# Kernel tuning notes

Hardware: AMD Instinct MI355X
Metric: run time of the kernel (lower is better)

## Reference

```python
import jax, jax.numpy as jnp
import numpy as np

B, T, C = 4, 2048, 1024
H, HS = 16, 64


def setup_inputs() -> dict:
    key = jax.random.key(0)
    ks = jax.random.split(key, 5)
    scale = (H * C) ** (-0.5)
    x = jax.random.normal(ks[0], (B, T, C), dtype=jnp.float32)
    Wk = jax.random.normal(ks[1], (H, C, HS), dtype=jnp.float32) * scale
    Wq = jax.random.normal(ks[2], (H, C, HS), dtype=jnp.float32) * scale
    Wv = jax.random.normal(ks[3], (H, C, HS), dtype=jnp.float32) * scale
    proj_w = jax.random.normal(ks[4], (C, C), dtype=jnp.float32) / C ** 0.5
    proj_b = jnp.zeros((C,), dtype=jnp.float32)
    return {"x": x, "Wk": Wk, "Wq": Wq, "Wv": Wv, "proj_w": proj_w, "proj_b": proj_b}


def reference(x, Wk, Wq, Wv, proj_w, proj_b):
    b, t, c = x.shape
    # per-head projections: (B,T,C) x (H,C,D) -> (B,H,T,D)
    q = jnp.einsum('btc,hcd->bhtd', x, Wq)
    k = jnp.einsum('btc,hcd->bhtd', x, Wk)
    v = jnp.einsum('btc,hcd->bhtd', x, Wv)
    # NOTE: original module does not scale by 1/sqrt(head_size)
    wei = jnp.einsum('bhtd,bhsd->bhts', q, k)  # (B,H,T,T)
    causal = jnp.tril(jnp.ones((t, t), dtype=bool))
    wei = jnp.where(causal, wei, -jnp.inf)
    wei = jax.nn.softmax(wei, axis=-1)
    out = jnp.einsum('bhts,bhsd->bhtd', wei, v)
    out = out.transpose(0, 2, 1, 3).reshape(b, t, c)  # concat heads
    return out @ proj_w + proj_b
```

## Files before the change

kernel.cpp:

```cpp
#include <hip/hip_runtime.h>

typedef unsigned short u16;
typedef u16 u16x4 __attribute__((ext_vector_type(4)));
typedef u16 u16x8 __attribute__((ext_vector_type(8)));
typedef unsigned u32x2 __attribute__((ext_vector_type(2)));
typedef __bf16 bf16x8 __attribute__((ext_vector_type(8)));
typedef float f32x4 __attribute__((ext_vector_type(4)));

#define DEV static __device__ __forceinline__

DEV u16 f2bf(float f) {
  union { float f; unsigned u; } v; v.f = f;
  return (u16)((v.u + 0x7FFFu + ((v.u >> 16) & 1u)) >> 16);
}

DEV unsigned pack2(float a, float b) {
  unsigned ua = __builtin_bit_cast(unsigned, a) + 0x8000u;
  unsigned ub = __builtin_bit_cast(unsigned, b) + 0x8000u;
  return (ua >> 16) | (ub & 0xFFFF0000u);
}

DEV void async16(const void* g, void* l) {
  __builtin_amdgcn_global_load_lds((const __attribute__((address_space(1))) void*)g,
                                   (__attribute__((address_space(3))) void*)l, 16, 0, 0);
}

DEV f32x4 mfma16(bf16x8 a, bf16x8 b, f32x4 c) {
  return __builtin_amdgcn_mfma_f32_16x16x32_bf16(a, b, c, 0, 0, 0);
}

DEV float exp2fast(float x) { return __builtin_amdgcn_exp2f(x); }

__global__ __launch_bounds__(256) void k_pack_x(const float* __restrict__ x,
                                                u16* __restrict__ o) {
  int i = (blockIdx.x * 256 + threadIdx.x) * 4;
  float4 v = *(const float4*)(x + i);
  u16x4 t = { f2bf(v.x), f2bf(v.y), f2bf(v.z), f2bf(v.w) };
  *(u16x4*)(o + i) = t;
}

__global__ __launch_bounds__(256) void k_tpack(const float* __restrict__ src,
                                               u16* __restrict__ dst,
                                               int rows, int cols, float scale) {
  __shared__ float t[64 * 72];
  const int tid = threadIdx.x;
  src += (size_t)blockIdx.z * rows * cols;
  dst += (size_t)blockIdx.z * rows * cols;
  const int c0 = blockIdx.x * 64, r0 = blockIdx.y * 64;
  const int rr = tid >> 2, cb = (tid & 3) * 16;
  const float* s = src + (size_t)(r0 + rr) * cols + c0 + cb;
  float4 v0 = *(const float4*)(s + 0);
  float4 v1 = *(const float4*)(s + 4);
  float4 v2 = *(const float4*)(s + 8);
  float4 v3 = *(const float4*)(s + 12);
  *(float4*)(t + rr * 72 + cb + 0)  = v0;
  *(float4*)(t + rr * 72 + cb + 4)  = v1;
  *(float4*)(t + rr * 72 + cb + 8)  = v2;
  *(float4*)(t + rr * 72 + cb + 12) = v3;
  __syncthreads();
  const int dd = tid >> 2, eb = (tid & 3) * 16;
  u16x8 o0, o1;
#pragma unroll
  for (int e = 0; e < 8; ++e) o0[e] = f2bf(t[(eb + e) * 72 + dd] * scale);
#pragma unroll
  for (int e = 0; e < 8; ++e) o1[e] = f2bf(t[(eb + 8 + e) * 72 + dd] * scale);
  u16* dp = dst + (size_t)(c0 + dd) * rows + r0 + eb;
  *(u16x8*)dp = o0;
  *(u16x8*)(dp + 8) = o1;
}

template <int MODE>
__global__ __launch_bounds__(256) void k_gemm(const u16* __restrict__ A,
                                              const u16* __restrict__ Bt,
                                              u16* __restrict__ qd,
                                              u16* __restrict__ kd,
                                              u16* __restrict__ vd,
                                              float* __restrict__ out,
                                              const float* __restrict__ bias) {
  __shared__ u16 As[128 * 32];
  __shared__ u16 Bs[128 * 32];
  const int tid = threadIdx.x;
  const int wave = tid >> 6, lane = tid & 63;
  const int quad = lane >> 4, l15 = lane & 15;
  const int wm = wave & 1, wn = wave >> 1;
  const size_t mb = blockIdx.y, nb = blockIdx.x;
  const u16* ga = A + (mb * 128 + (tid >> 2)) * 1024 + (tid & 3) * 8;
  const u16* gb = Bt + (nb * 128 + (tid >> 2)) * 1024 + (tid & 3) * 8;
  f32x4 acc[4][4] = {};
  for (int k0 = 0; k0 < 1024; k0 += 32) {
    async16(ga,             As + wave * 512);
    async16(ga + 64 * 1024, As + 2048 + wave * 512);
    async16(gb,             Bs + wave * 512);
    async16(gb + 64 * 1024, Bs + 2048 + wave * 512);
    ga += 32; gb += 32;
    __syncthreads();
    bf16x8 af[4], bf[4];
#pragma unroll
    for (int i = 0; i < 4; ++i)
      af[i] = *(const bf16x8*)(As + (wm * 64 + i * 16 + l15) * 32 + quad * 8);
#pragma unroll
    for (int j = 0; j < 4; ++j)
      bf[j] = *(const bf16x8*)(Bs + (wn * 64 + j * 16 + l15) * 32 + quad * 8);
#pragma unroll
    for (int i = 0; i < 4; ++i)
#pragma unroll
      for (int j = 0; j < 4; ++j)
        acc[i][j] = mfma16(af[i], bf[j], acc[i][j]);
    __syncthreads();
  }
  const size_t m0 = mb * 128 + wm * 64;
  const int n0 = (int)nb * 128 + wn * 64;
  if (MODE == 0) {
#pragma unroll
    for (int j = 0; j < 4; ++j) {
      const int n = n0 + j * 16 + l15;
      const int p = n >> 10, hh = (n >> 6) & 15, d = n & 63;
      if (p == 2) {
#pragma unroll
        for (int i = 0; i < 4; ++i) {
          const size_t m = m0 + i * 16 + quad * 4;
          const size_t bb = m >> 11, tt = m & 2047;
          u16x4 pk = { f2bf(acc[i][j][0]), f2bf(acc[i][j][1]),
                       f2bf(acc[i][j][2]), f2bf(acc[i][j][3]) };
          *(u16x4*)(vd + ((bb * 16 + hh) * 64 + d) * 2048 + tt) = pk;
        }
      } else {
        u16* dst = (p == 0) ? qd : kd;
#pragma unroll
        for (int i = 0; i < 4; ++i)
#pragma unroll
          for (int r = 0; r < 4; ++r) {
            const size_t m = m0 + i * 16 + quad * 4 + r;
            const size_t bb = m >> 11, tt = m & 2047;
            dst[((bb * 16 + hh) * 2048 + tt) * 64 + d] = f2bf(acc[i][j][r]);
          }
      }
    }
  } else {
#pragma unroll
    for (int j = 0; j < 4; ++j) {
      const int n = n0 + j * 16 + l15;
      const float bv = bias[n];
#pragma unroll
      for (int i = 0; i < 4; ++i)
#pragma unroll
        for (int r = 0; r < 4; ++r) {
          const size_t m = m0 + i * 16 + quad * 4 + r;
          out[m * 1024 + n] = acc[i][j][r] + bv;
        }
    }
  }
}

__global__ __launch_bounds__(256) void k_attn(const u16* __restrict__ Qg,
                                              const u16* __restrict__ Kg,
                                              const u16* __restrict__ Vtg,
                                              u16* __restrict__ Og) {
  __shared__ u16 Kbuf[2 * 4096];
  __shared__ u16 Vbuf[2 * 4096];
  __shared__ u16 Pbuf[4 * 32 * 72];
  const int tid = threadIdx.x;
  const int wave = tid >> 6, lane = tid & 63;
  const int quad = lane >> 4, l15 = lane & 15;
  const int quad4 = quad * 4, quad8 = quad * 8;
  const int bh = blockIdx.x;
  const int qpair = blockIdx.y;
  const u16* kg = Kg + (size_t)bh * 2048 * 64;
  const u16* vg = Vtg + (size_t)bh * 64 * 2048;
  u16* Pw = Pbuf + wave * (32 * 72);
  const int b = bh >> 4, h = bh & 15;

  const int lrow = lane >> 3;
  const int lchunk = ((lane & 7) ^ lrow) << 3;
  const u16* kst = kg + (size_t)(wave * 16 + lrow) * 64 + lchunk;
  const u16* vst = vg + (size_t)(wave * 16 + lrow) * 2048 + lchunk;
  u16* kdst0 = Kbuf + wave * 1024;
  u16* vdst0 = Vbuf + wave * 1024;

  const int rowoff = l15 * 64;
  const int swz0 = ((0 + quad) ^ (l15 & 7)) << 3;
  const int swz1 = ((4 + quad) ^ (l15 & 7)) << 3;

  for (int half = 0; half < 2; ++half) {
    const int qb = half ? (15 - qpair) : qpair;
    const int qlo = qb * 128 + wave * 32;
    const int ntw = 2 * qb + 1 + (wave >> 1);
    const int ntb = 2 * qb + 2;
    const u16* qg = Qg + ((size_t)bh * 2048 + (size_t)qb * 128) * 64;

    bf16x8 qf[2][2];
#pragma unroll
    for (int i = 0; i < 2; ++i)
#pragma unroll
      for (int c = 0; c < 2; ++c)
        qf[i][c] = *(const bf16x8*)(qg + (size_t)(wave * 32 + i * 16 + l15) * 64 +
                                    c * 32 + quad8);

    f32x4 oacc[2][4] = {};
    float lsum[2] = {0.f, 0.f};

    {
      async16(kst, kdst0);
      async16(kst + 512, kdst0 + 512);
      async16(vst, vdst0);
      async16(vst + 16384, vdst0 + 512);
    }

    for (int it = 0; it < ntb; ++it) {
      __syncthreads();

      if (it + 1 < ntb) {
        const int buf = (it + 1) & 1;
        const size_t s0 = (size_t)(it + 1) * 64;
        async16(kst + s0 * 64,        kdst0 + buf * 4096);
        async16(kst + s0 * 64 + 512,  kdst0 + buf * 4096 + 512);
        async16(vst + s0,             vdst0 + buf * 4096);
        async16(vst + s0 + 16384,     vdst0 + buf * 4096 + 512);
      }

      if (it < ntw) {
        const int s0 = it * 64;
        const u16* Kb = Kbuf + (it & 1) * 4096;
        const u16* Vb = Vbuf + (it & 1) * 4096;

        f32x4 sacc[4][2] = {};
#pragma unroll
        for (int j = 0; j < 4; ++j) {
          bf16x8 kf0 = *(const bf16x8*)(Kb + j * 1024 + rowoff + swz0);
          bf16x8 kf1 = *(const bf16x8*)(Kb + j * 1024 + rowoff + swz1);
          sacc[j][0] = mfma16(kf0, qf[0][0], sacc[j][0]);
          sacc[j][0] = mfma16(kf1, qf[0][1], sacc[j][0]);
          sacc[j][1] = mfma16(kf0, qf[1][0], sacc[j][1]);
          sacc[j][1] = mfma16(kf1, qf[1][1], sacc[j][1]);
        }

#pragma unroll
        for (int j = 0; j < 4; ++j)
#pragma unroll
          for (int i = 0; i < 2; ++i)
#pragma unroll
            for (int r = 0; r < 4; ++r)
              sacc[j][i][r] = exp2fast(sacc[j][i][r]);

        if (it == ntw - 1) {
#pragma unroll
          for (int j = 0; j < 4; ++j)
#pragma unroll
            for (int i = 0; i < 2; ++i)
#pragma unroll
              for (int r = 0; r < 4; ++r)
                if (s0 + j * 16 + quad4 + r > qlo + i * 16 + l15) sacc[j][i][r] = 0.f;
        }

#pragma unroll
        for (int j = 0; j < 4; ++j)
#pragma unroll
          for (int i = 0; i < 2; ++i) {
            lsum[i] += (sacc[j][i][0] + sacc[j][i][1]) +
                       (sacc[j][i][2] + sacc[j][i][3]);
            u32x2 pk = { pack2(sacc[j][i][0], sacc[j][i][1]),
                         pack2(sacc[j][i][2], sacc[j][i][3]) };
            *(u32x2*)(Pw + (i * 16 + l15) * 72 + j * 16 + quad4) = pk;
          }

        bf16x8 pa[2][2];
#pragma unroll
        for (int i = 0; i < 2; ++i)
#pragma unroll
          for (int c = 0; c < 2; ++c)
            pa[i][c] = *(const bf16x8*)(Pw + (i * 16 + l15) * 72 + c * 32 + quad8);

#pragma unroll
        for (int n = 0; n < 4; ++n) {
          bf16x8 vf0 = *(const bf16x8*)(Vb + n * 1024 + rowoff + swz0);
          bf16x8 vf1 = *(const bf16x8*)(Vb + n * 1024 + rowoff + swz1);
          oacc[0][n] = mfma16(pa[0][0], vf0, oacc[0][n]);
          oacc[0][n] = mfma16(pa[0][1], vf1, oacc[0][n]);
          oacc[1][n] = mfma16(pa[1][0], vf0, oacc[1][n]);
          oacc[1][n] = mfma16(pa[1][1], vf1, oacc[1][n]);
        }
      }
    }

#pragma unroll
    for (int i = 0; i < 2; ++i) {
      lsum[i] += __shfl_xor(lsum[i], 16, 64);
      lsum[i] += __shfl_xor(lsum[i], 32, 64);
    }
#pragma unroll
    for (int i = 0; i < 2; ++i)
#pragma unroll
      for (int r = 0; r < 4; ++r) {
        const float inv = 1.0f / __shfl(lsum[i], quad4 + r, 16);
        const size_t t = (size_t)qb * 128 + wave * 32 + i * 16 + quad4 + r;
#pragma unroll
        for (int n = 0; n < 4; ++n)
          Og[((size_t)b * 2048 + t) * 1024 + h * 64 + n * 16 + l15] =
              f2bf(oacc[i][n][r] * inv);
      }

    __syncthreads();
  }
}

extern "C" void kernel_launch(void* const* d_in, const int* in_sizes, int n_in,
                              void* d_out, int out_size, void* d_ws, size_t ws_size,
                              hipStream_t stream) {
  const float* x  = (const float*)d_in[0];
  const float* Wk = (const float*)d_in[1];
  const float* Wq = (const float*)d_in[2];
  const float* Wv = (const float*)d_in[3];
  const float* pw = (const float*)d_in[4];
  const float* pb = (const float*)d_in[5];
  float* out = (float*)d_out;
  char* ws = (char*)d_ws;

  u16* xb  = (u16*)(ws + 0);
  u16* wT  = (u16*)(ws + 16777216);
  u16* pwT = (u16*)(ws + 23068672);
  u16* q   = (u16*)(ws + 25165824);
  u16* kb  = (u16*)(ws + 41943040);
  u16* vt  = (u16*)(ws + 58720256);
  u16* att = (u16*)(ws + 0);

  const float LOG2E = 1.44269504088896340736f;
  k_pack_x<<<8192, 256, 0, stream>>>(x, xb);
  k_tpack<<<dim3(1, 16, 16), 256, 0, stream>>>(Wq, wT + 0,           1024, 64, LOG2E);
  k_tpack<<<dim3(1, 16, 16), 256, 0, stream>>>(Wk, wT + 1024 * 1024, 1024, 64, 1.0f);
  k_tpack<<<dim3(1, 16, 16), 256, 0, stream>>>(Wv, wT + 2048 * 1024, 1024, 64, 1.0f);
  k_tpack<<<dim3(16, 16, 1), 256, 0, stream>>>(pw, pwT, 1024, 1024, 1.0f);
  k_gemm<0><<<dim3(24, 64), 256, 0, stream>>>(xb, wT, q, kb, vt, nullptr, nullptr);
  k_attn<<<dim3(64, 8), 256, 0, stream>>>(q, kb, vt, att);
  k_gemm<1><<<dim3(8, 64), 256, 0, stream>>>(att, pwT, nullptr, nullptr, nullptr, out, pb);
}
```

Before: 269.3 us.

## Process four query blocks per attention workgroup sharing one K/V stream

Each attention workgroup now handles four causal-balanced query blocks (a, a+4, 11-a, 15-a) at once instead of two sequentially. Every K/V tile is loaded from global memory and LDS a single time and reused across all four query blocks, cutting redundant K/V traffic. The cost is half as many workgroups (256 over 256 CUs), heavy register pressure from four sets of accumulators and Q fragments (hence launch_bounds(256,1)), and possible spills or lower occupancy.

After: 285.8 us. +6.1%, slower.

```diff
diff --git a/kernel.cpp b/kernel.cpp
--- a/kernel.cpp
+++ b/kernel.cpp
@@ -152,10 +152,10 @@
   }
 }
 
-__global__ __launch_bounds__(256) void k_attn(const u16* __restrict__ Qg,
-                                              const u16* __restrict__ Kg,
-                                              const u16* __restrict__ Vtg,
-                                              u16* __restrict__ Og) {
+__global__ __launch_bounds__(256, 1) void k_attn(const u16* __restrict__ Qg,
+                                                 const u16* __restrict__ Kg,
+                                                 const u16* __restrict__ Vtg,
+                                                 u16* __restrict__ Og) {
   __shared__ u16 Kbuf[2 * 4096];
   __shared__ u16 Vbuf[2 * 4096];
   __shared__ u16 Pbuf[4 * 32 * 72];
@@ -164,9 +164,11 @@
   const int quad = lane >> 4, l15 = lane & 15;
   const int quad4 = quad * 4, quad8 = quad * 8;
   const int bh = blockIdx.x;
-  const int qpair = blockIdx.y;
+  const int a = blockIdx.y;
+  const int qbs[4] = { a, a + 4, 11 - a, 15 - a };
   const u16* kg = Kg + (size_t)bh * 2048 * 64;
   const u16* vg = Vtg + (size_t)bh * 64 * 2048;
+  const u16* qgb = Qg + (size_t)bh * 2048 * 64;
   u16* Pw = Pbuf + wave * (32 * 72);
   const int b = bh >> 4, h = bh & 15;
 
@@ -181,57 +183,65 @@
   const int swz0 = ((0 + quad) ^ (l15 & 7)) << 3;
   const int swz1 = ((4 + quad) ^ (l15 & 7)) << 3;
 
-  for (int half = 0; half < 2; ++half) {
-    const int qb = half ? (15 - qpair) : qpair;
-    const int qlo = qb * 128 + wave * 32;
-    const int ntw = 2 * qb + 1 + (wave >> 1);
-    const int ntb = 2 * qb + 2;
-    const u16* qg = Qg + ((size_t)bh * 2048 + (size_t)qb * 128) * 64;
-
-    bf16x8 qf[2][2];
+  bf16x8 qf[4][2][2];
+  int ntw[4], qlo[4];
+#pragma unroll
+  for (int z = 0; z < 4; ++z) {
+    qlo[z] = qbs[z] * 128 + wave * 32;
+    ntw[z] = 2 * qbs[z] + 1 + (wave >> 1);
 #pragma unroll
     for (int i = 0; i < 2; ++i)
 #pragma unroll
       for (int c = 0; c < 2; ++c)
-        qf[i][c] = *(const bf16x8*)(qg + (size_t)(wave * 32 + i * 16 + l15) * 64 +
-                                    c * 32 + quad8);
-
-    f32x4 oacc[2][4] = {};
-    float lsum[2] = {0.f, 0.f};
-
-    {
-      async16(kst, kdst0);
-      async16(kst + 512, kdst0 + 512);
-      async16(vst, vdst0);
-      async16(vst + 16384, vdst0 + 512);
-    }
-
-    for (int it = 0; it < ntb; ++it) {
-      __syncthreads();
-
-      if (it + 1 < ntb) {
-        const int buf = (it + 1) & 1;
-        const size_t s0 = (size_t)(it + 1) * 64;
-        async16(kst + s0 * 64,        kdst0 + buf * 4096);
-        async16(kst + s0 * 64 + 512,  kdst0 + buf * 4096 + 512);
-        async16(vst + s0,             vdst0 + buf * 4096);
-        async16(vst + s0 + 16384,     vdst0 + buf * 4096 + 512);
-      }
-
-      if (it < ntw) {
-        const int s0 = it * 64;
-        const u16* Kb = Kbuf + (it & 1) * 4096;
-        const u16* Vb = Vbuf + (it & 1) * 4096;
-
+        qf[z][i][c] = *(const bf16x8*)(qgb +
+            (size_t)(qbs[z] * 128 + wave * 32 + i * 16 + l15) * 64 + c * 32 + quad8);
+  }
+
+  f32x4 oacc[4][2][4] = {};
+  float lsum[4][2] = {};
+
+  const int ntb = 2 * (15 - a) + 2;
+
+  async16(kst, kdst0);
+  async16(kst + 512, kdst0 + 512);
+  async16(vst, vdst0);
+  async16(vst + 16384, vdst0 + 512);
+
+  for (int it = 0; it < ntb; ++it) {
+    __syncthreads();
+
+    if (it + 1 < ntb) {
+      const int buf = (it + 1) & 1;
+      const size_t s0n = (size_t)(it + 1) * 64;
+      async16(kst + s0n * 64,       kdst0 + buf * 4096);
+      async16(kst + s0n * 64 + 512, kdst0 + buf * 4096 + 512);
+      async16(vst + s0n,            vdst0 + buf * 4096);
+      async16(vst + s0n + 16384,    vdst0 + buf * 4096 + 512);
+    }
+
+    const int s0 = it * 64;
+    const u16* Kb = Kbuf + (it & 1) * 4096;
+    const u16* Vb = Vbuf + (it & 1) * 4096;
+
+    bf16x8 kf[4][2], vf[4][2];
+#pragma unroll
+    for (int j = 0; j < 4; ++j) {
+      kf[j][0] = *(const bf16x8*)(Kb + j * 1024 + rowoff + swz0);
+      kf[j][1] = *(const bf16x8*)(Kb + j * 1024 + rowoff + swz1);
+      vf[j][0] = *(const bf16x8*)(Vb + j * 1024 + rowoff + swz0);
+      vf[j][1] = *(const bf16x8*)(Vb + j * 1024 + rowoff + swz1);
+    }
+
+#pragma unroll
+    for (int z = 0; z < 4; ++z) {
+      if (it < ntw[z]) {
         f32x4 sacc[4][2] = {};
 #pragma unroll
         for (int j = 0; j < 4; ++j) {
-          bf16x8 kf0 = *(const bf16x8*)(Kb + j * 1024 + rowoff + swz0);
-          bf16x8 kf1 = *(const bf16x8*)(Kb + j * 1024 + rowoff + swz1);
-          sacc[j][0] = mfma16(kf0, qf[0][0], sacc[j][0]);
-          sacc[j][0] = mfma16(kf1, qf[0][1], sacc[j][0]);
-          sacc[j][1] = mfma16(kf0, qf[1][0], sacc[j][1]);
-          sacc[j][1] = mfma16(kf1, qf[1][1], sacc[j][1]);
+          sacc[j][0] = mfma16(kf[j][0], qf[z][0][0], sacc[j][0]);
+          sacc[j][0] = mfma16(kf[j][1], qf[z][0][1], sacc[j][0]);
+          sacc[j][1] = mfma16(kf[j][0], qf[z][1][0], sacc[j][1]);
+          sacc[j][1] = mfma16(kf[j][1], qf[z][1][1], sacc[j][1]);
         }
 
 #pragma unroll
@@ -242,22 +252,23 @@
             for (int r = 0; r < 4; ++r)
               sacc[j][i][r] = exp2fast(sacc[j][i][r]);
 
-        if (it == ntw - 1) {
+        if (it == ntw[z] - 1) {
 #pragma unroll
           for (int j = 0; j < 4; ++j)
 #pragma unroll
             for (int i = 0; i < 2; ++i)
 #pragma unroll
               for (int r = 0; r < 4; ++r)
-                if (s0 + j * 16 + quad4 + r > qlo + i * 16 + l15) sacc[j][i][r] = 0.f;
+                if (s0 + j * 16 + quad4 + r > qlo[z] + i * 16 + l15)
+                  sacc[j][i][r] = 0.f;
         }
 
 #pragma unroll
         for (int j = 0; j < 4; ++j)
 #pragma unroll
           for (int i = 0; i < 2; ++i) {
-            lsum[i] += (sacc[j][i][0] + sacc[j][i][1]) +
-                       (sacc[j][i][2] + sacc[j][i][3]);
+            lsum[z][i] += (sacc[j][i][0] + sacc[j][i][1]) +
+                          (sacc[j][i][2] + sacc[j][i][3]);
             u32x2 pk = { pack2(sacc[j][i][0], sacc[j][i][1]),
                          pack2(sacc[j][i][2], sacc[j][i][3]) };
             *(u32x2*)(Pw + (i * 16 + l15) * 72 + j * 16 + quad4) = pk;
@@ -272,34 +283,33 @@
 
 #pragma unroll
         for (int n = 0; n < 4; ++n) {
-          bf16x8 vf0 = *(const bf16x8*)(Vb + n * 1024 + rowoff + swz0);
-          bf16x8 vf1 = *(const bf16x8*)(Vb + n * 1024 + rowoff + swz1);
-          oacc[0][n] = mfma16(pa[0][0], vf0, oacc[0][n]);
-          oacc[0][n] = mfma16(pa[0][1], vf1, oacc[0][n]);
-          oacc[1][n] = mfma16(pa[1][0], vf0, oacc[1][n]);
-          oacc[1][n] = mfma16(pa[1][1], vf1, oacc[1][n]);
+          oacc[z][0][n] = mfma16(pa[0][0], vf[n][0], oacc[z][0][n]);
+          oacc[z][0][n] = mfma16(pa[0][1], vf[n][1], oacc[z][0][n]);
+          oacc[z][1][n] = mfma16(pa[1][0], vf[n][0], oacc[z][1][n]);
+          oacc[z][1][n] = mfma16(pa[1][1], vf[n][1], oacc[z][1][n]);
         }
       }
     }
-
+  }
+
+#pragma unroll
+  for (int z = 0; z < 4; ++z) {
 #pragma unroll
     for (int i = 0; i < 2; ++i) {
-      lsum[i] += __shfl_xor(lsum[i], 16, 64);
-      lsum[i] += __shfl_xor(lsum[i], 32, 64);
+      lsum[z][i] += __shfl_xor(lsum[z][i], 16, 64);
+      lsum[z][i] += __shfl_xor(lsum[z][i], 32, 64);
     }
 #pragma unroll
     for (int i = 0; i < 2; ++i)
 #pragma unroll
       for (int r = 0; r < 4; ++r) {
-        const float inv = 1.0f / __shfl(lsum[i], quad4 + r, 16);
-        const size_t t = (size_t)qb * 128 + wave * 32 + i * 16 + quad4 + r;
+        const float inv = 1.0f / __shfl(lsum[z][i], quad4 + r, 16);
+        const size_t t = (size_t)qbs[z] * 128 + wave * 32 + i * 16 + quad4 + r;
 #pragma unroll
         for (int n = 0; n < 4; ++n)
           Og[((size_t)b * 2048 + t) * 1024 + h * 64 + n * 16 + l15] =
-              f2bf(oacc[i][n][r] * inv);
+              f2bf(oacc[z][i][n][r] * inv);
       }
-
-    __syncthreads();
   }
 }
 
@@ -330,6 +340,6 @@
   k_tpack<<<dim3(1, 16, 16), 256, 0, stream>>>(Wv, wT + 2048 * 1024, 1024, 64, 1.0f);
   k_tpack<<<dim3(16, 16, 1), 256, 0, stream>>>(pw, pwT, 1024, 1024, 1.0f);
   k_gemm<0><<<dim3(24, 64), 256, 0, stream>>>(xb, wT, q, kb, vt, nullptr, nullptr);
-  k_attn<<<dim3(64, 8), 256, 0, stream>>>(q, kb, vt, att);
+  k_attn<<<dim3(64, 4), 256, 0, stream>>>(q, kb, vt, att);
   k_gemm<1><<<dim3(8, 64), 256, 0, stream>>>(att, pwT, nullptr, nullptr, nullptr, out, pb);
 }
```
